# Kernel tuning notes

Hardware: AMD Instinct MI355X
Metric: run time of the kernel (lower is better)

## Reference

```python
import jax, jax.numpy as jnp
import numpy as np

EMBED = 64
HEADS = 8
N, S = 8, 1024


def setup_inputs() -> dict:
    key = jax.random.key(0)
    ks = jax.random.split(key, 8)
    scale = 1.0 / np.sqrt(EMBED)
    return {
        "values": jax.random.normal(ks[0], (N, S, EMBED), dtype=jnp.float32),
        "keys": jax.random.normal(ks[1], (N, S, EMBED), dtype=jnp.float32),
        "queries": jax.random.normal(ks[2], (N, S, EMBED), dtype=jnp.float32),
        # per-head projection weights, torch Linear convention: y = x @ W.T
        "Wv": jax.random.normal(ks[3], (HEADS, EMBED, EMBED), dtype=jnp.float32) * scale,
        "Wk": jax.random.normal(ks[4], (HEADS, EMBED, EMBED), dtype=jnp.float32) * scale,
        "Wq": jax.random.normal(ks[5], (HEADS, EMBED, EMBED), dtype=jnp.float32) * scale,
        "Wout": jax.random.normal(ks[6], (EMBED, HEADS * EMBED), dtype=jnp.float32) * (1.0 / np.sqrt(HEADS * EMBED)),
        "bout": jnp.zeros((EMBED,), dtype=jnp.float32),
    }


def reference(values, keys, queries, Wv, Wk, Wq, Wout, bout):
    d = queries.shape[-1]
    # Batched per-head projections (each head keeps full embed dim, per the module)
    v = jnp.einsum("nkd,hed->nhke", values, Wv)   # [N,H,K,D]
    k = jnp.einsum("nkd,hed->nhke", keys, Wk)     # [N,H,K,D]
    q = jnp.einsum("nqd,hed->nhqe", queries, Wq)  # [N,H,Q,D]
    energy = jnp.einsum("nhqd,nhkd->nhqk", q, k)
    attn = jax.nn.softmax(energy / jnp.sqrt(jnp.asarray(d, energy.dtype)), axis=-1)  # [N,H,Q,K]
    head_out = jnp.einsum("nhqk,nhkd->nhqd", attn, v)  # [N,H,Q,D]
    # torch.cat(output_heads, dim=2) == transpose heads next to feature then flatten
    nN, nH, nQ, nD = head_out.shape
    cat = jnp.transpose(head_out, (0, 2, 1, 3)).reshape(nN, nQ, nH * nD)  # [N,Q,H*D]
    out = cat @ Wout.T + bout  # [N,Q,D]
    return out, attn
```

## Files before the change

### kernel.cpp

```cpp
#include <hip/hip_runtime.h>

typedef __bf16 bf16x8 __attribute__((ext_vector_type(8)));
typedef __bf16 bf16x4 __attribute__((ext_vector_type(4)));
typedef float  f32x4  __attribute__((ext_vector_type(4)));

#define MFMA16(a, b, c) __builtin_amdgcn_mfma_f32_16x16x32_bf16((a), (b), (c), 0, 0, 0)

constexpr int N_ = 8, H_ = 8, S_ = 1024, D_ = 64;

__global__ __launch_bounds__(256) void proj_kernel(
    const float* __restrict__ Xq, const float* __restrict__ Xk,
    const float* __restrict__ Xv,
    const float* __restrict__ Wq, const float* __restrict__ Wk,
    const float* __restrict__ Wv,
    unsigned short* __restrict__ qb_, unsigned short* __restrict__ kb_,
    unsigned short* __restrict__ vtb_)
{
    __shared__ __bf16 T[64 * 72];

    const int which = blockIdx.y;
    const float* X = (which == 0) ? Xq : (which == 1) ? Xk : Xv;
    const float* W = (which == 0) ? Wq : (which == 1) ? Wk : Wv;

    const int b   = blockIdx.x;
    const int st  = b & 15;
    const int h   = (b >> 4) & 7;
    const int n   = b >> 7;
    const int s0  = st * 64;
    const int nh  = n * H_ + h;
    const int tid = threadIdx.x;
    const int w = tid >> 6, lane = tid & 63;
    const int l16 = lane & 15, quad = lane >> 4;

    const float* xrow = X + (size_t)(n * S_ + s0 + w * 16 + l16) * D_;
    bf16x8 a[2];
#pragma unroll
    for (int half = 0; half < 2; ++half) {
        const float* p = xrow + half * 32 + quad * 8;
        f32x4 x0 = *(const f32x4*)p;
        f32x4 x1 = *(const f32x4*)(p + 4);
#pragma unroll
        for (int j = 0; j < 4; ++j) { a[half][j] = (__bf16)x0[j]; a[half][4 + j] = (__bf16)x1[j]; }
    }

#pragma unroll
    for (int et = 0; et < 4; ++et) {
        const int e0 = et * 16;
        f32x4 acc = {0.f, 0.f, 0.f, 0.f};
#pragma unroll
        for (int half = 0; half < 2; ++half) {
            const float* wp = W + ((size_t)(h * 64 + e0 + l16)) * 64 + half * 32 + quad * 8;
            f32x4 x0 = *(const f32x4*)wp;
            f32x4 x1 = *(const f32x4*)(wp + 4);
            bf16x8 bf;
#pragma unroll
            for (int j = 0; j < 4; ++j) { bf[j] = (__bf16)x0[j]; bf[4 + j] = (__bf16)x1[j]; }
            acc = MFMA16(a[half], bf, acc);
        }
#pragma unroll
        for (int r = 0; r < 4; ++r) {
            const int sl = w * 16 + quad * 4 + r;
            const int e  = e0 + l16;
            const __bf16 v = (__bf16)acc[r];
            if (which == 2) T[e * 72 + sl] = v;
            else            T[sl * 72 + e] = v;
        }
    }
    __syncthreads();

    if (which == 0) {
        const int row = tid >> 2, seg = tid & 3;
        const bf16x8 d0 = *(const bf16x8*)&T[row * 72 + seg * 16];
        const bf16x8 d1 = *(const bf16x8*)&T[row * 72 + seg * 16 + 8];
        __bf16* dst = (__bf16*)qb_ + ((size_t)nh * S_ + s0 + row) * D_ + seg * 16;
        *(bf16x8*)dst = d0;
        *(bf16x8*)(dst + 8) = d1;
    } else if (which == 1) {
#pragma unroll
        for (int cc = 0; cc < 2; ++cc) {
            const int c   = tid + cc * 256;
            const int ktl = c >> 7;
            const int h2  = (c >> 6) & 1;
            const int ll  = c & 63;
            const bf16x8 d = *(const bf16x8*)&T[(ktl * 16 + (ll & 15)) * 72 + h2 * 32 + (ll >> 4) * 8];
            __bf16* dst = (__bf16*)kb_ +
                (((size_t)(nh * 64 + st * 4 + ktl) * 2 + h2) * 512 + ll * 8);
            *(bf16x8*)dst = d;
        }
    } else {
#pragma unroll
        for (int cc = 0; cc < 2; ++cc) {
            const int c   = tid + cc * 256;
            const int chl = c >> 8;
            const int et  = (c >> 6) & 3;
            const int lv  = c & 63;
            const bf16x8 d = *(const bf16x8*)&T[(et * 16 + (lv & 15)) * 72 + chl * 32 + (lv >> 4) * 8];
            __bf16* dst = (__bf16*)vtb_ + (size_t)nh * 65536 +
                ((size_t)(st * 2 + chl) * 2048 + et * 512 + lv * 8);
            *(bf16x8*)dst = d;
        }
    }
}

__global__ __launch_bounds__(256, 8) void attn_kernel(
    const unsigned short* __restrict__ qb_, const unsigned short* __restrict__ kb_,
    const unsigned short* __restrict__ vtb_,
    float* __restrict__ attn_out, unsigned short* __restrict__ catb_)
{
    __shared__ float Sred[4 * 16];
    __shared__ float Ored[2 * 16 * 68];

    const __bf16* qb  = (const __bf16*)qb_;
    const __bf16* kb  = (const __bf16*)kb_;
    const __bf16* vtb = (const __bf16*)vtb_;
    __bf16* catb = (__bf16*)catb_;

    const int bid = blockIdx.x;
    const int b   = (bid & 7) * 256 + (bid >> 3);
    const int qt  = b & 31;
    const int h   = (b >> 5) & 7;
    const int n   = b >> 8;
    const int nh  = n * H_ + h;
    const int q0  = qt * 32;

    const int tid = threadIdx.x;
    const int w = tid >> 6, lane = tid & 63;
    const int l16 = lane & 15, quad = lane >> 4;
    const int rw = w & 1;
    const int kw = w >> 1;
    const int k0 = kw * 512;

    const __bf16* qbase = qb + ((size_t)(nh * S_ + q0 + rw * 16 + l16)) * D_;
    const bf16x8 aq0 = *(const bf16x8*)(qbase + quad * 8);
    const bf16x8 aq1 = *(const bf16x8*)(qbase + 32 + quad * 8);

    const __bf16* kfrag = kb + ((size_t)(nh * 64 + kw * 32)) * 1024 + lane * 8;

    float ssum = 0.f;
#pragma unroll 4
    for (int kt = 0; kt < 32; ++kt) {
        const __bf16* kp = kfrag + kt * 1024;
        const bf16x8 b0 = *(const bf16x8*)kp;
        const bf16x8 b1 = *(const bf16x8*)(kp + 512);
        f32x4 c = {0.f, 0.f, 0.f, 0.f};
        c = MFMA16(b0, aq0, c);
        c = MFMA16(b1, aq1, c);
#pragma unroll
        for (int r = 0; r < 4; ++r) ssum += __expf(c[r] * 0.125f);
    }
    ssum += __shfl_xor(ssum, 16);
    ssum += __shfl_xor(ssum, 32);
    if (lane < 16) Sred[w * 16 + lane] = ssum;
    __syncthreads();
    const float inv = 1.0f / (Sred[w * 16 + l16] + Sred[(w ^ 2) * 16 + l16]);

    float* abase = attn_out + ((size_t)(nh * S_ + q0 + rw * 16 + l16)) * S_ + k0;
    const __bf16* vfrag = vtb + (size_t)nh * 65536 + (size_t)kw * 16 * 2048 + lane * 8;

    const int lo_addr = (((quad & 1) * 2) * 16 + l16) * 4;
    const int hi_addr = lo_addr + 64;
    const bool hiq = (quad & 2) != 0;

    f32x4 acc[4] = {{0.f,0.f,0.f,0.f},{0.f,0.f,0.f,0.f},{0.f,0.f,0.f,0.f},{0.f,0.f,0.f,0.f}};

#pragma unroll 2
    for (int ch = 0; ch < 16; ++ch) {
        unsigned Wt[2][2];
#pragma unroll
        for (int t = 0; t < 2; ++t) {
            const int kt = ch * 2 + t;
            const __bf16* kp = kfrag + kt * 1024;
            const bf16x8 b0 = *(const bf16x8*)kp;
            const bf16x8 b1 = *(const bf16x8*)(kp + 512);
            f32x4 c = {0.f, 0.f, 0.f, 0.f};
            c = MFMA16(b0, aq0, c);
            c = MFMA16(b1, aq1, c);
            float p[4];
#pragma unroll
            for (int r = 0; r < 4; ++r) p[r] = __expf(c[r] * 0.125f) * inv;
#pragma unroll
            for (int pr = 0; pr < 2; ++pr) {
                const __bf16 ha = (__bf16)p[2 * pr], hb = (__bf16)p[2 * pr + 1];
                const unsigned ua = *(const unsigned short*)&ha;
                const unsigned ub = *(const unsigned short*)&hb;
                Wt[t][pr] = ua | (ub << 16);
            }
        }
        const int s00 = __builtin_amdgcn_ds_bpermute(lo_addr, (int)Wt[0][0]);
        const int s10 = __builtin_amdgcn_ds_bpermute(lo_addr, (int)Wt[1][0]);
        const int s01 = __builtin_amdgcn_ds_bpermute(lo_addr, (int)Wt[0][1]);
        const int s11 = __builtin_amdgcn_ds_bpermute(lo_addr, (int)Wt[1][1]);
        const int s02 = __builtin_amdgcn_ds_bpermute(hi_addr, (int)Wt[0][0]);
        const int s12 = __builtin_amdgcn_ds_bpermute(hi_addr, (int)Wt[1][0]);
        const int s03 = __builtin_amdgcn_ds_bpermute(hi_addr, (int)Wt[0][1]);
        const int s13 = __builtin_amdgcn_ds_bpermute(hi_addr, (int)Wt[1][1]);
        union { bf16x8 v; unsigned u[4]; } pf;
        pf.u[0] = (unsigned)(hiq ? s10 : s00);
        pf.u[1] = (unsigned)(hiq ? s11 : s01);
        pf.u[2] = (unsigned)(hiq ? s12 : s02);
        pf.u[3] = (unsigned)(hiq ? s13 : s03);

#pragma unroll
        for (int et = 0; et < 4; ++et) {
            const bf16x8 bv = *(const bf16x8*)(vfrag + ch * 2048 + et * 512);
            acc[et] = MFMA16(pf.v, bv, acc[et]);
        }

        f32x4 f0, f1;
#pragma unroll
        for (int j = 0; j < 4; ++j) { f0[j] = (float)pf.v[j]; f1[j] = (float)pf.v[4 + j]; }
        float* ap = abase + ch * 32 + quad * 8;
        *(f32x4*)ap = f0;
        *(f32x4*)(ap + 4) = f1;
    }

    __syncthreads();
    if (kw == 1) {
#pragma unroll
        for (int et = 0; et < 4; ++et)
#pragma unroll
            for (int r = 0; r < 4; ++r)
                Ored[rw * (16 * 68) + (quad * 4 + r) * 68 + et * 16 + l16] = acc[et][r];
    }
    __syncthreads();
    if (kw == 0) {
#pragma unroll
        for (int r = 0; r < 4; ++r) {
            const int s = q0 + rw * 16 + quad * 4 + r;
            __bf16* cp = catb + ((size_t)n * S_ + s) * (H_ * D_) + h * D_ + l16;
#pragma unroll
            for (int et = 0; et < 4; ++et) {
                const float o = acc[et][r] +
                    Ored[rw * (16 * 68) + (quad * 4 + r) * 68 + et * 16 + l16];
                cp[et * 16] = (__bf16)o;
            }
        }
    }
}

__global__ __launch_bounds__(256) void outproj_kernel(
    const unsigned short* __restrict__ catb_, const float* __restrict__ Wout,
    const float* __restrict__ bout, float* __restrict__ out)
{
    __shared__ float R[4 * 16 * 68];

    const __bf16* catb = (const __bf16*)catb_;
    const int r0  = blockIdx.x * 16;
    const int tid = threadIdx.x;
    const int w = tid >> 6, lane = tid & 63;
    const int l16 = lane & 15, quad = lane >> 4;
    const int k0 = w * 128;

    const __bf16* arow  = catb + (size_t)(r0 + l16) * 512 + k0 + quad * 8;
    const float*  wbase = Wout + (size_t)l16 * 512 + k0 + quad * 8;

    f32x4 acc[4] = {{0.f,0.f,0.f,0.f},{0.f,0.f,0.f,0.f},{0.f,0.f,0.f,0.f},{0.f,0.f,0.f,0.f}};

#pragma unroll
    for (int kc = 0; kc < 4; ++kc) {
        const bf16x8 af = *(const bf16x8*)(arow + kc * 32);
#pragma unroll
        for (int et = 0; et < 4; ++et) {
            const float* wp = wbase + (size_t)et * 16 * 512 + kc * 32;
            f32x4 x0 = *(const f32x4*)wp;
            f32x4 x1 = *(const f32x4*)(wp + 4);
            bf16x8 bf;
#pragma unroll
            for (int j = 0; j < 4; ++j) { bf[j] = (__bf16)x0[j]; bf[4 + j] = (__bf16)x1[j]; }
            acc[et] = MFMA16(af, bf, acc[et]);
        }
    }
#pragma unroll
    for (int et = 0; et < 4; ++et)
#pragma unroll
        for (int r = 0; r < 4; ++r)
            R[w * (16 * 68) + (quad * 4 + r) * 68 + et * 16 + l16] = acc[et][r];
    __syncthreads();

    const int row = tid >> 4, c0 = (tid & 15) * 4;
    f32x4 s = *(const f32x4*)&R[row * 68 + c0];
#pragma unroll
    for (int wv = 1; wv < 4; ++wv) s += *(const f32x4*)&R[wv * (16 * 68) + row * 68 + c0];
    s += *(const f32x4*)(bout + c0);
    *(f32x4*)(out + (size_t)(r0 + row) * 64 + c0) = s;
}

extern "C" void kernel_launch(void* const* d_in, const int* in_sizes, int n_in,
                              void* d_out, int out_size, void* d_ws, size_t ws_size,
                              hipStream_t stream)
{
    const float* values  = (const float*)d_in[0];
    const float* keys    = (const float*)d_in[1];
    const float* queries = (const float*)d_in[2];
    const float* Wv      = (const float*)d_in[3];
    const float* Wk      = (const float*)d_in[4];
    const float* Wq      = (const float*)d_in[5];
    const float* Wout    = (const float*)d_in[6];
    const float* bout    = (const float*)d_in[7];

    float* out  = (float*)d_out;
    float* attn = out + (size_t)N_ * S_ * D_;

    const size_t nelem = (size_t)N_ * H_ * S_ * D_;
    unsigned short* qb   = (unsigned short*)d_ws;
    unsigned short* kb   = qb  + nelem;
    unsigned short* vtb  = kb  + nelem;
    unsigned short* catb = vtb + nelem;

    proj_kernel<<<dim3(N_ * H_ * (S_ / 64), 3), 256, 0, stream>>>(
        queries, keys, values, Wq, Wk, Wv, qb, kb, vtb);
    attn_kernel<<<N_ * H_ * (S_ / 32), 256, 0, stream>>>(qb, kb, vtb, attn, catb);
    outproj_kernel<<<(N_ * S_) / 16, 256, 0, stream>>>(catb, Wout, bout, out);
}
```

Measured before the change: 392.9 us.

## Fuse softmax-sum pass into PV loop, buffer probabilities in registers, defer normalization

Removes the separate first pass that recomputed QK^T only to get the softmax denominators. The kernel now accumulates unnormalized exp values into the PV accumulators and keeps the bf16 probabilities in a 64-entry register buffer. After the row sums are reduced, it writes the normalized attention matrix with nontemporal stores and rescales the output accumulators. This halves the QK MFMA and exp work and K loads, but raises register pressure, so launch bounds drop from 8 to 4 blocks. The written attn values are bf16-rounded before normalization rather than after, which slightly changes rounding.

```diff
diff --git a/kernel.cpp b/kernel.cpp
--- a/kernel.cpp
+++ b/kernel.cpp
@@ -102,7 +102,7 @@
     }
 }
 
-__global__ __launch_bounds__(256, 8) void attn_kernel(
+__global__ __launch_bounds__(256, 4) void attn_kernel(
     const unsigned short* __restrict__ qb_, const unsigned short* __restrict__ kb_,
     const unsigned short* __restrict__ vtb_,
     float* __restrict__ attn_out, unsigned short* __restrict__ catb_)
@@ -135,35 +135,17 @@
     const bf16x8 aq1 = *(const bf16x8*)(qbase + 32 + quad * 8);
 
     const __bf16* kfrag = kb + ((size_t)(nh * 64 + kw * 32)) * 1024 + lane * 8;
-
-    float ssum = 0.f;
-#pragma unroll 4
-    for (int kt = 0; kt < 32; ++kt) {
-        const __bf16* kp = kfrag + kt * 1024;
-        const bf16x8 b0 = *(const bf16x8*)kp;
-        const bf16x8 b1 = *(const bf16x8*)(kp + 512);
-        f32x4 c = {0.f, 0.f, 0.f, 0.f};
-        c = MFMA16(b0, aq0, c);
-        c = MFMA16(b1, aq1, c);
-#pragma unroll
-        for (int r = 0; r < 4; ++r) ssum += __expf(c[r] * 0.125f);
-    }
-    ssum += __shfl_xor(ssum, 16);
-    ssum += __shfl_xor(ssum, 32);
-    if (lane < 16) Sred[w * 16 + lane] = ssum;
-    __syncthreads();
-    const float inv = 1.0f / (Sred[w * 16 + l16] + Sred[(w ^ 2) * 16 + l16]);
-
-    float* abase = attn_out + ((size_t)(nh * S_ + q0 + rw * 16 + l16)) * S_ + k0;
     const __bf16* vfrag = vtb + (size_t)nh * 65536 + (size_t)kw * 16 * 2048 + lane * 8;
 
     const int lo_addr = (((quad & 1) * 2) * 16 + l16) * 4;
     const int hi_addr = lo_addr + 64;
     const bool hiq = (quad & 2) != 0;
 
+    unsigned Pbuf[16][4];
+    float ssum = 0.f;
     f32x4 acc[4] = {{0.f,0.f,0.f,0.f},{0.f,0.f,0.f,0.f},{0.f,0.f,0.f,0.f},{0.f,0.f,0.f,0.f}};
 
-#pragma unroll 2
+#pragma unroll
     for (int ch = 0; ch < 16; ++ch) {
         unsigned Wt[2][2];
 #pragma unroll
@@ -177,7 +159,7 @@
             c = MFMA16(b1, aq1, c);
             float p[4];
 #pragma unroll
-            for (int r = 0; r < 4; ++r) p[r] = __expf(c[r] * 0.125f) * inv;
+            for (int r = 0; r < 4; ++r) { p[r] = __expf(c[r] * 0.125f); ssum += p[r]; }
 #pragma unroll
             for (int pr = 0; pr < 2; ++pr) {
                 const __bf16 ha = (__bf16)p[2 * pr], hb = (__bf16)p[2 * pr + 1];
@@ -199,20 +181,49 @@
         pf.u[1] = (unsigned)(hiq ? s11 : s01);
         pf.u[2] = (unsigned)(hiq ? s12 : s02);
         pf.u[3] = (unsigned)(hiq ? s13 : s03);
+        Pbuf[ch][0] = pf.u[0]; Pbuf[ch][1] = pf.u[1];
+        Pbuf[ch][2] = pf.u[2]; Pbuf[ch][3] = pf.u[3];
 
 #pragma unroll
         for (int et = 0; et < 4; ++et) {
             const bf16x8 bv = *(const bf16x8*)(vfrag + ch * 2048 + et * 512);
             acc[et] = MFMA16(pf.v, bv, acc[et]);
         }
-
+    }
+
+    ssum += __shfl_xor(ssum, 16);
+    ssum += __shfl_xor(ssum, 32);
+    if (lane < 16) Sred[w * 16 + lane] = ssum;
+    __syncthreads();
+    const float inv = 1.0f / (Sred[w * 16 + l16] + Sred[(w ^ 2) * 16 + l16]);
+
+    float* abase = attn_out + ((size_t)(nh * S_ + q0 + rw * 16 + l16)) * S_ + k0;
+#pragma unroll
+    for (int ch = 0; ch < 16; ++ch) {
+        union { bf16x8 v; unsigned u[4]; } pf;
+        pf.u[0] = Pbuf[ch][0]; pf.u[1] = Pbuf[ch][1];
+        pf.u[2] = Pbuf[ch][2]; pf.u[3] = Pbuf[ch][3];
         f32x4 f0, f1;
 #pragma unroll
-        for (int j = 0; j < 4; ++j) { f0[j] = (float)pf.v[j]; f1[j] = (float)pf.v[4 + j]; }
+        for (int j = 0; j < 4; ++j) {
+            f0[j] = (float)pf.v[j] * inv;
+            f1[j] = (float)pf.v[4 + j] * inv;
+        }
         float* ap = abase + ch * 32 + quad * 8;
-        *(f32x4*)ap = f0;
-        *(f32x4*)(ap + 4) = f1;
-    }
+        __builtin_nontemporal_store(f0, (f32x4*)ap);
+        __builtin_nontemporal_store(f1, (f32x4*)(ap + 4));
+    }
+
+    float invr[4];
+#pragma unroll
+    for (int r = 0; r < 4; ++r) {
+        const int row = quad * 4 + r;
+        invr[r] = 1.0f / (Sred[w * 16 + row] + Sred[(w ^ 2) * 16 + row]);
+    }
+#pragma unroll
+    for (int et = 0; et < 4; ++et)
+#pragma unroll
+        for (int r = 0; r < 4; ++r) acc[et][r] *= invr[r];
 
     __syncthreads();
     if (kw == 1) {
```

After: 432.3 us. +10.0%, slower.
